# Optimization experiments

Measured on AMD Instinct MI355X. Metric: run time of the kernel, lower is better.

## Reference

```python
import jax, jax.numpy as jnp
import numpy as np
from jax.ops import segment_sum, segment_max

N, E, G = 20000, 100000, 16
TILE, EMB, HID, OUT, FEAT, HEADS = 32, 128, 256, 512, 512, 8
SLOPE = 0.2


def setup_inputs() -> dict:
    key = jax.random.key(0)
    ks = jax.random.split(key, 20)
    def gn(k, shape, fan_in):
        return jax.random.normal(k, shape, jnp.float32) * (1.0 / np.sqrt(fan_in))
    return {
        "x": jax.random.normal(ks[0], (N, TILE), jnp.float32),
        "edge_index": jax.random.randint(ks[1], (2, E), 0, N, jnp.int32),
        "batch": jnp.sort(jax.random.randint(ks[2], (N,), 0, G, jnp.int32)),
        "W0": gn(ks[3], (TILE, EMB), TILE), "b0": jnp.zeros((EMB,), jnp.float32),
        "W1": gn(ks[4], (EMB, HEADS * HID), EMB),
        "a1s": gn(ks[5], (HEADS, HID), HID), "a1d": gn(ks[6], (HEADS, HID), HID),
        "b1": jnp.zeros((HEADS * HID,), jnp.float32),
        "W2": gn(ks[7], (HEADS * HID, HEADS * HID), HEADS * HID),
        "a2s": gn(ks[8], (HEADS, HID), HID), "a2d": gn(ks[9], (HEADS, HID), HID),
        "b2": jnp.zeros((HEADS * HID,), jnp.float32),
        "W3": gn(ks[10], (HEADS * HID, OUT), HEADS * HID),
        "a3s": gn(ks[11], (1, OUT), OUT), "a3d": gn(ks[12], (1, OUT), OUT),
        "b3": jnp.zeros((OUT,), jnp.float32),
        "Wf": gn(ks[13], (OUT, FEAT), OUT), "bf": jnp.zeros((FEAT,), jnp.float32),
    }


def gat_conv(x, src, dst, W, a_s, a_d, b, heads, ch, n):
    # PyG GATConv: linear, per-edge additive attention, segment softmax over dst, scatter-add
    h = (x @ W).reshape(n, heads, ch)                       # [N,H,C]
    e_src = jnp.einsum("nhc,hc->nh", h, a_s)                 # [N,H]
    e_dst = jnp.einsum("nhc,hc->nh", h, a_d)
    e = jax.nn.leaky_relu(e_src[src] + e_dst[dst], SLOPE)    # [E,H]
    m = segment_max(e, dst, num_segments=n)                  # [N,H]
    m = jax.lax.stop_gradient(jnp.where(jnp.isfinite(m), m, 0.0))
    ex = jnp.exp(e - m[dst])
    den = segment_sum(ex, dst, num_segments=n)
    alpha = ex / (den[dst] + 1e-16)                          # [E,H]
    out = segment_sum(h[src] * alpha[..., None], dst, num_segments=n)  # [N,H,C]
    return out.reshape(n, heads * ch) + b


def reference(x, edge_index, batch, W0, b0, W1, a1s, a1d, b1, W2, a2s, a2d, b2,
              W3, a3s, a3d, b3, Wf, bf):
    loop = jnp.arange(N, dtype=edge_index.dtype)             # PyG adds self-loops by default
    src = jnp.concatenate([edge_index[0], loop])
    dst = jnp.concatenate([edge_index[1], loop])
    h = jax.nn.leaky_relu(x @ W0 + b0, SLOPE)
    h = jax.nn.leaky_relu(gat_conv(h, src, dst, W1, a1s, a1d, b1, HEADS, HID, N), SLOPE)
    h = jax.nn.leaky_relu(gat_conv(h, src, dst, W2, a2s, a2d, b2, HEADS, HID, N), SLOPE)
    h = jax.nn.leaky_relu(gat_conv(h, src, dst, W3, a3s, a3d, b3, 1, OUT, N), SLOPE)
    sums = segment_sum(h, batch, num_segments=G)             # global_mean_pool
    cnt = segment_sum(jnp.ones((N,), h.dtype), batch, num_segments=G)
    mean = sums / jnp.maximum(cnt, 1.0)[:, None]
    return jax.nn.leaky_relu(mean @ Wf + bf, SLOPE)
```

## Files before the change

### kernel.cpp

```cpp
#include <hip/hip_runtime.h>
#include <hip/hip_bf16.h>

#define N_NODES 20000
#define N_EDGES 100000
#define ET (N_EDGES + N_NODES)
#define G_GRAPHS 16
#define SLOPE 0.2f

using short8  = __attribute__((ext_vector_type(8))) short;
using floatx4 = __attribute__((ext_vector_type(4))) float;

__device__ __forceinline__ float lrelu(float x) { return x > 0.f ? x : SLOPE * x; }

__device__ __forceinline__ float b2f(unsigned short u) {
    union { unsigned int i; float f; } v; v.i = ((unsigned int)u) << 16; return v.f;
}
__device__ __forceinline__ unsigned short f2b(float f) {
    union { float f; unsigned int i; } v; v.f = f;
    unsigned int i = v.i;
    return (unsigned short)((i + 0x7fffu + ((i >> 16) & 1u)) >> 16);
}

__device__ __forceinline__ void gld16(const void* g, void* l) {
    __builtin_amdgcn_global_load_lds((const __attribute__((address_space(1))) void*)g,
                                     (__attribute__((address_space(3))) void*)l, 16, 0, 0);
}

__device__ int dev_lower_bound(const int* a, int n, int key) {
    int lo = 0, hi = n;
    while (lo < hi) { int mid = (lo + hi) >> 1; if (a[mid] < key) lo = mid + 1; else hi = mid; }
    return lo;
}

__global__ void zero_kernel(int* __restrict__ p, int n) {
    int i = blockIdx.x * blockDim.x + threadIdx.x;
    if (i < n) p[i] = 0;
}

__global__ void count_kernel(const int* __restrict__ ei, int* __restrict__ counts) {
    int e = blockIdx.x * blockDim.x + threadIdx.x;
    if (e >= ET) return;
    int dst = (e < N_EDGES) ? ei[N_EDGES + e] : (e - N_EDGES);
    atomicAdd(&counts[dst], 1);
}

__global__ void scan_kernel(const int* __restrict__ counts, int* __restrict__ row_ptr) {
    __shared__ int sums[256];
    int t = threadIdx.x;
    const int CH = (N_NODES + 255) / 256;
    int base = t * CH;
    int s = 0;
    for (int i = 0; i < CH; i++) { int idx = base + i; if (idx < N_NODES) s += counts[idx]; }
    sums[t] = s;
    __syncthreads();
    for (int off = 1; off < 256; off <<= 1) {
        int v = (t >= off) ? sums[t - off] : 0;
        __syncthreads();
        sums[t] += v;
        __syncthreads();
    }
    int run = (t == 0) ? 0 : sums[t - 1];
    for (int i = 0; i < CH; i++) {
        int idx = base + i;
        if (idx < N_NODES) { row_ptr[idx] = run; run += counts[idx]; }
    }
    if (t == 255) row_ptr[N_NODES] = run;
}

__global__ void fill_kernel(const int* __restrict__ ei, const int* __restrict__ row_ptr,
                            int* __restrict__ fill_cnt, int* __restrict__ col) {
    int e = blockIdx.x * blockDim.x + threadIdx.x;
    if (e >= ET) return;
    int src, dst;
    if (e < N_EDGES) { src = ei[e]; dst = ei[N_EDGES + e]; }
    else             { src = dst = e - N_EDGES; }
    int pos = atomicAdd(&fill_cnt[dst], 1);
    col[row_ptr[dst] + pos] = src;
}

__global__ void transpose_kernel(const float* __restrict__ W, unsigned short* __restrict__ Wt,
                                 int K, int N) {
    __shared__ float tile[32][33];
    int bn = blockIdx.x * 32, bk = blockIdx.y * 32;
    int tx = threadIdx.x & 31, ty = threadIdx.x >> 5;
#pragma unroll
    for (int p = 0; p < 32; p += 8)
        tile[ty + p][tx] = W[(size_t)(bk + ty + p) * N + bn + tx];
    __syncthreads();
#pragma unroll
    for (int p = 0; p < 32; p += 8)
        Wt[(size_t)(bn + ty + p) * K + bk + tx] = f2b(tile[tx][ty + p]);
}

__global__ void gemm0_kernel(const float* __restrict__ x, const float* __restrict__ W0,
                             const float* __restrict__ b0, unsigned short* __restrict__ h0) {
    __shared__ float xr[32];
    int n = blockIdx.x, t = threadIdx.x;
    if (t < 32) xr[t] = x[n * 32 + t];
    __syncthreads();
    float acc = 0.f;
#pragma unroll
    for (int k = 0; k < 32; k++) acc += xr[k] * W0[k * 128 + t];
    h0[(size_t)n * 128 + t] = f2b(lrelu(acc + b0[t]));
}

__global__ void wes_kernel(const float* __restrict__ W1, const float* __restrict__ a1s,
                           const float* __restrict__ a1d, float* __restrict__ w_es,
                           float* __restrict__ w_ed) {
    int hd = blockIdx.x;
    int k  = threadIdx.x;
    const float* w  = W1 + (size_t)k * 2048 + hd * 256;
    const float* as_ = a1s + hd * 256;
    const float* ad_ = a1d + hd * 256;
    float s1 = 0.f, s2 = 0.f;
    for (int c = 0; c < 256; c++) { float wv = w[c]; s1 += wv * as_[c]; s2 += wv * ad_[c]; }
    w_es[k * 8 + hd] = s1;
    w_ed[k * 8 + hd] = s2;
}

__global__ void es1_kernel(const unsigned short* __restrict__ h0, const float* __restrict__ w_es,
                           const float* __restrict__ w_ed, float* __restrict__ es,
                           float* __restrict__ ed) {
    int n = blockIdx.x, t = threadIdx.x;
    int hd = t >> 5, l = t & 31;
    uint2 u = *(const uint2*)&h0[(size_t)n * 128 + l * 4];
    float x0 = b2f((unsigned short)(u.x & 0xffff)), x1 = b2f((unsigned short)(u.x >> 16));
    float x2 = b2f((unsigned short)(u.y & 0xffff)), x3 = b2f((unsigned short)(u.y >> 16));
    int k0 = l * 4;
    float s1 = x0 * w_es[(k0 + 0) * 8 + hd] + x1 * w_es[(k0 + 1) * 8 + hd] +
               x2 * w_es[(k0 + 2) * 8 + hd] + x3 * w_es[(k0 + 3) * 8 + hd];
    float s2 = x0 * w_ed[(k0 + 0) * 8 + hd] + x1 * w_ed[(k0 + 1) * 8 + hd] +
               x2 * w_ed[(k0 + 2) * 8 + hd] + x3 * w_ed[(k0 + 3) * 8 + hd];
    for (int m = 16; m >= 1; m >>= 1) { s1 += __shfl_xor(s1, m); s2 += __shfl_xor(s2, m); }
    if (l == 0) { es[n * 8 + hd] = s1; ed[n * 8 + hd] = s2; }
}

__global__ __launch_bounds__(256) void agg1_wave(const unsigned short* __restrict__ h0,
                                                 const float* __restrict__ es,
                                                 const float* __restrict__ ed,
                                                 const int* __restrict__ row_ptr,
                                                 const int* __restrict__ col,
                                                 unsigned short* __restrict__ outp) {
    int wv = threadIdx.x >> 6, l = threadIdx.x & 63;
    int v = blockIdx.x * 4 + wv;
    if (v >= N_NODES) return;
    int rs = row_ptr[v], deg = row_ptr[v + 1] - rs;
    float edv[8], den[8], a0[8], a1[8];
#pragma unroll
    for (int hd = 0; hd < 8; hd++) { edv[hd] = ed[v * 8 + hd]; den[hd] = 0.f; a0[hd] = 0.f; a1[hd] = 0.f; }
    int sN = (deg > 0) ? col[rs] : 0;
    for (int e = 0; e < deg; e++) {
        int s = sN;
        if (e + 1 < deg) sN = col[rs + e + 1];
        unsigned int u = *(const unsigned int*)&h0[(size_t)s * 128 + l * 2];
        float x0 = b2f((unsigned short)(u & 0xffff)), x1 = b2f((unsigned short)(u >> 16));
#pragma unroll
        for (int hd = 0; hd < 8; hd++) {
            float a = __expf(lrelu(es[s * 8 + hd] + edv[hd]));
            den[hd] += a;
            a0[hd] += a * x0;
            a1[hd] += a * x1;
        }
    }
#pragma unroll
    for (int hd = 0; hd < 8; hd++) {
        float inv = 1.f / (den[hd] + 1e-16f);
        unsigned int o = (unsigned int)f2b(a0[hd] * inv) | ((unsigned int)f2b(a1[hd] * inv) << 16);
        *(unsigned int*)&outp[(size_t)v * 1024 + hd * 128 + l * 2] = o;
    }
}

__global__ __launch_bounds__(256) void gemm_mfma(const unsigned short* __restrict__ A,
                                                 const unsigned short* __restrict__ Bt,
                                                 unsigned short* __restrict__ C,
                                                 int M, int N, int K) {
    __shared__ __align__(16) unsigned short As[128][32];
    __shared__ __align__(16) unsigned short Bs[128][32];
    int t = threadIdx.x;
    int w = t >> 6, l = t & 63;
    int r0 = blockIdx.y * 128, c0 = blockIdx.x * 128;
    int wr = (w >> 1) * 64, wc = (w & 1) * 64;
    int lrow = l >> 2;
    int gcb  = (l & 3) ^ ((l >> 3) & 3);
    int m16 = l & 15, qb = l >> 4;
    int sw  = (m16 >> 1) & 3;
    int roff = ((qb ^ sw) * 8);
    floatx4 acc[4][4] = {};

    for (int k0 = 0; k0 < K; k0 += 32) {
        __syncthreads();
#pragma unroll
        for (int q = 0; q < 2; q++) {
            int row = w * 32 + q * 16 + lrow;
            int ga = min(r0 + row, M - 1);
            gld16(A + (size_t)ga * K + k0 + gcb * 8, &As[w * 32 + q * 16][0]);
            gld16(Bt + (size_t)(c0 + row) * K + k0 + gcb * 8, &Bs[w * 32 + q * 16][0]);
        }
        __syncthreads();
        short8 af[4], bfr[4];
#pragma unroll
        for (int i = 0; i < 4; i++) af[i] = *(const short8*)&As[wr + i * 16 + m16][roff];
#pragma unroll
        for (int j = 0; j < 4; j++) bfr[j] = *(const short8*)&Bs[wc + j * 16 + m16][roff];
#pragma unroll
        for (int i = 0; i < 4; i++)
#pragma unroll
            for (int j = 0; j < 4; j++)
                acc[i][j] = __builtin_amdgcn_mfma_f32_16x16x32_bf16(bfr[j], af[i], acc[i][j], 0, 0, 0);
    }
    int quad = l >> 4;
#pragma unroll
    for (int i = 0; i < 4; i++) {
        int r = r0 + wr + i * 16 + m16;
        if (r < M) {
#pragma unroll
            for (int j = 0; j < 4; j++) {
                int c = c0 + wc + j * 16 + quad * 4;
                ushort4 o = make_ushort4(f2b(acc[i][j][0]), f2b(acc[i][j][1]),
                                         f2b(acc[i][j][2]), f2b(acc[i][j][3]));
                *(ushort4*)&C[(size_t)r * N + c] = o;
            }
        }
    }
}

__global__ __launch_bounds__(256) void gemm_mfma_h1(const unsigned short* __restrict__ A,
                                                    const unsigned short* __restrict__ Bt,
                                                    const float* __restrict__ bias,
                                                    unsigned short* __restrict__ C,
                                                    int M) {
    const int N = 2048, K = 128;
    __shared__ __align__(16) unsigned short As[128][32];
    __shared__ __align__(16) unsigned short Bs[128][32];
    int t = threadIdx.x;
    int w = t >> 6, l = t & 63;
    int r0 = blockIdx.y * 128, c0 = blockIdx.x * 128;
    int wr = (w >> 1) * 64, wc = (w & 1) * 64;
    int lrow = l >> 2;
    int gcb  = (l & 3) ^ ((l >> 3) & 3);
    int m16 = l & 15, qb = l >> 4;
    int sw  = (m16 >> 1) & 3;
    int roff = ((qb ^ sw) * 8);
    int aoff = (c0 >> 8) * 128;
    floatx4 acc[4][4] = {};

    for (int k0 = 0; k0 < K; k0 += 32) {
        __syncthreads();
#pragma unroll
        for (int q = 0; q < 2; q++) {
            int row = w * 32 + q * 16 + lrow;
            int ga = min(r0 + row, M - 1);
            gld16(A + (size_t)ga * 1024 + aoff + k0 + gcb * 8, &As[w * 32 + q * 16][0]);
            gld16(Bt + (size_t)(c0 + row) * K + k0 + gcb * 8, &Bs[w * 32 + q * 16][0]);
        }
        __syncthreads();
        short8 af[4], bfr[4];
#pragma unroll
        for (int i = 0; i < 4; i++) af[i] = *(const short8*)&As[wr + i * 16 + m16][roff];
#pragma unroll
        for (int j = 0; j < 4; j++) bfr[j] = *(const short8*)&Bs[wc + j * 16 + m16][roff];
#pragma unroll
        for (int i = 0; i < 4; i++)
#pragma unroll
            for (int j = 0; j < 4; j++)
                acc[i][j] = __builtin_amdgcn_mfma_f32_16x16x32_bf16(bfr[j], af[i], acc[i][j], 0, 0, 0);
    }
    int quad = l >> 4;
#pragma unroll
    for (int i = 0; i < 4; i++) {
        int r = r0 + wr + i * 16 + m16;
        if (r < M) {
#pragma unroll
            for (int j = 0; j < 4; j++) {
                int c = c0 + wc + j * 16 + quad * 4;
                ushort4 o = make_ushort4(f2b(lrelu(acc[i][j][0] + bias[c + 0])),
                                         f2b(lrelu(acc[i][j][1] + bias[c + 1])),
                                         f2b(lrelu(acc[i][j][2] + bias[c + 2])),
                                         f2b(lrelu(acc[i][j][3] + bias[c + 3])));
                *(ushort4*)&C[(size_t)r * N + c] = o;
            }
        }
    }
}

__global__ void att8_kernel(const unsigned short* __restrict__ h, const float* __restrict__ a_s,
                            const float* __restrict__ a_d, float* __restrict__ es,
                            float* __restrict__ ed) {
    int n = blockIdx.x, t = threadIdx.x;
    int hd = t >> 5, l = t & 31;
    const unsigned short* hr = h + (size_t)n * 2048 + hd * 256 + l * 8;
    const float* as_ = a_s + hd * 256 + l * 8;
    const float* ad_ = a_d + hd * 256 + l * 8;
    uint4 u = *(const uint4*)hr;
    float v[8] = { b2f((unsigned short)(u.x & 0xffff)), b2f((unsigned short)(u.x >> 16)),
                   b2f((unsigned short)(u.y & 0xffff)), b2f((unsigned short)(u.y >> 16)),
                   b2f((unsigned short)(u.z & 0xffff)), b2f((unsigned short)(u.z >> 16)),
                   b2f((unsigned short)(u.w & 0xffff)), b2f((unsigned short)(u.w >> 16)) };
    float s1 = 0.f, s2 = 0.f;
#pragma unroll
    for (int j = 0; j < 8; j++) { s1 += v[j] * as_[j]; s2 += v[j] * ad_[j]; }
    for (int m = 16; m >= 1; m >>= 1) { s1 += __shfl_xor(s1, m); s2 += __shfl_xor(s2, m); }
    if (l == 0) { es[n * 8 + hd] = s1; ed[n * 8 + hd] = s2; }
}

__global__ void att1_kernel(const unsigned short* __restrict__ h, const float* __restrict__ a_s,
                            const float* __restrict__ a_d, float* __restrict__ es,
                            float* __restrict__ ed) {
    int n = blockIdx.x, l = threadIdx.x;
    const unsigned short* hr = h + (size_t)n * 512 + l * 8;
    const float* as_ = a_s + l * 8;
    const float* ad_ = a_d + l * 8;
    uint4 u = *(const uint4*)hr;
    float v[8] = { b2f((unsigned short)(u.x & 0xffff)), b2f((unsigned short)(u.x >> 16)),
                   b2f((unsigned short)(u.y & 0xffff)), b2f((unsigned short)(u.y >> 16)),
                   b2f((unsigned short)(u.z & 0xffff)), b2f((unsigned short)(u.z >> 16)),
                   b2f((unsigned short)(u.w & 0xffff)), b2f((unsigned short)(u.w >> 16)) };
    float s1 = 0.f, s2 = 0.f;
#pragma unroll
    for (int j = 0; j < 8; j++) { s1 += v[j] * as_[j]; s2 += v[j] * ad_[j]; }
    for (int m = 32; m >= 1; m >>= 1) { s1 += __shfl_xor(s1, m); s2 += __shfl_xor(s2, m); }
    if (l == 0) { es[n] = s1; ed[n] = s2; }
}

template <int H, int C>
__global__ __launch_bounds__(256) void agg_wave(const unsigned short* __restrict__ hmid,
                                                const float* __restrict__ es,
                                                const float* __restrict__ ed,
                                                const int* __restrict__ row_ptr,
                                                const int* __restrict__ col,
                                                const float* __restrict__ bias,
                                                unsigned short* __restrict__ out) {
    constexpr int HC = H * C;
    constexpr int CH = HC / 512;
    int wv = threadIdx.x >> 6, l = threadIdx.x & 63;
    int v = blockIdx.x * 4 + wv;
    if (v >= N_NODES) return;
    int rs = row_ptr[v], deg = row_ptr[v + 1] - rs;
    int hd[CH];
    float edv[CH], den[CH], acc[CH][8];
#pragma unroll
    for (int c = 0; c < CH; c++) {
        hd[c] = (c * 512 + l * 8) / C;
        edv[c] = ed[v * H + hd[c]];
        den[c] = 0.f;
#pragma unroll
        for (int k = 0; k < 8; k++) acc[c][k] = 0.f;
    }
    int sN = (deg > 0) ? col[rs] : 0;
    for (int e = 0; e < deg; e++) {
        int s = sN;
        if (e + 1 < deg) sN = col[rs + e + 1];
        const unsigned short* hr = hmid + (size_t)s * HC + l * 8;
        uint4 u[CH];
#pragma unroll
        for (int c = 0; c < CH; c++) u[c] = *(const uint4*)(hr + c * 512);
        float ex[CH];
#pragma unroll
        for (int c = 0; c < CH; c++) {
            ex[c] = __expf(lrelu(es[s * H + hd[c]] + edv[c]));
            den[c] += ex[c];
        }
#pragma unroll
        for (int c = 0; c < CH; c++) {
            float a = ex[c];
            acc[c][0] += a * b2f((unsigned short)(u[c].x & 0xffff));
            acc[c][1] += a * b2f((unsigned short)(u[c].x >> 16));
            acc[c][2] += a * b2f((unsigned short)(u[c].y & 0xffff));
            acc[c][3] += a * b2f((unsigned short)(u[c].y >> 16));
            acc[c][4] += a * b2f((unsigned short)(u[c].z & 0xffff));
            acc[c][5] += a * b2f((unsigned short)(u[c].z >> 16));
            acc[c][6] += a * b2f((unsigned short)(u[c].w & 0xffff));
            acc[c][7] += a * b2f((unsigned short)(u[c].w >> 16));
        }
    }
#pragma unroll
    for (int c = 0; c < CH; c++) {
        float inv = 1.f / (den[c] + 1e-16f);
        unsigned short o[8];
#pragma unroll
        for (int k = 0; k < 8; k++)
            o[k] = f2b(lrelu(acc[c][k] * inv + bias[c * 512 + l * 8 + k]));
        *(uint4*)&out[(size_t)v * HC + c * 512 + l * 8] = *(const uint4*)o;
    }
}

__global__ void pool_kernel(const unsigned short* __restrict__ h3, const int* __restrict__ batch,
                            float* __restrict__ msum) {
    int b0 = blockIdx.x * 128, t = threadIdx.x;
    int nend = min(b0 + 128, N_NODES);
    int curg = batch[b0];
    float s0 = 0.f, s1 = 0.f;
    for (int n = b0; n < nend; n++) {
        int g = batch[n];
        if (g != curg) {
            atomicAdd(&msum[curg * 512 + t * 2], s0);
            atomicAdd(&msum[curg * 512 + t * 2 + 1], s1);
            s0 = s1 = 0.f; curg = g;
        }
        unsigned int u = *(const unsigned int*)&h3[(size_t)n * 512 + t * 2];
        s0 += b2f((unsigned short)(u & 0xffff));
        s1 += b2f((unsigned short)(u >> 16));
    }
    atomicAdd(&msum[curg * 512 + t * 2], s0);
    atomicAdd(&msum[curg * 512 + t * 2 + 1], s1);
}

__global__ void final_kernel(const float* __restrict__ msum, const int* __restrict__ batch,
                             const float* __restrict__ Wf, const float* __restrict__ bf,
                             float* __restrict__ out) {
    int g = blockIdx.x, t = threadIdx.x;
    __shared__ float mr[512];
    __shared__ float sinv;
    if (t == 0) {
        int st = dev_lower_bound(batch, N_NODES, g);
        int en = dev_lower_bound(batch, N_NODES, g + 1);
        sinv = 1.f / fmaxf((float)(en - st), 1.f);
    }
    __syncthreads();
    for (int c = t; c < 512; c += 256) mr[c] = msum[g * 512 + c] * sinv;
    __syncthreads();
    for (int j = t; j < 512; j += 256) {
        float s = 0.f;
        for (int k = 0; k < 512; k++) s += mr[k] * Wf[k * 512 + j];
        out[g * 512 + j] = lrelu(s + bf[j]);
    }
}

extern "C" void kernel_launch(void* const* d_in, const int* in_sizes, int n_in,
                              void* d_out, int out_size, void* d_ws, size_t ws_size,
                              hipStream_t stream) {
    const float* x   = (const float*)d_in[0];
    const int*   ei  = (const int*)d_in[1];
    const int*   bat = (const int*)d_in[2];
    const float* W0  = (const float*)d_in[3];
    const float* b0  = (const float*)d_in[4];
    const float* W1  = (const float*)d_in[5];
    const float* a1s = (const float*)d_in[6];
    const float* a1d = (const float*)d_in[7];
    const float* b1  = (const float*)d_in[8];
    const float* W2  = (const float*)d_in[9];
    const float* a2s = (const float*)d_in[10];
    const float* a2d = (const float*)d_in[11];
    const float* b2  = (const float*)d_in[12];
    const float* W3  = (const float*)d_in[13];
    const float* a3s = (const float*)d_in[14];
    const float* a3d = (const float*)d_in[15];
    const float* b3  = (const float*)d_in[16];
    const float* Wf  = (const float*)d_in[17];
    const float* bf  = (const float*)d_in[18];
    float* out = (float*)d_out;

    char* p = (char*)d_ws;
    unsigned short* bufA = (unsigned short*)p; p += (size_t)N_NODES * 2048 * 2;
    unsigned short* bufB = (unsigned short*)p; p += (size_t)N_NODES * 2048 * 2;
    unsigned short* h0   = (unsigned short*)p; p += (size_t)N_NODES * 128 * 2;
    unsigned short* W1t  = (unsigned short*)p; p += (size_t)2048 * 128 * 2;
    unsigned short* W2t  = (unsigned short*)p; p += (size_t)2048 * 2048 * 2;
    unsigned short* W3t  = (unsigned short*)p; p += (size_t)512 * 2048 * 2;
    float* es   = (float*)p; p += (size_t)N_NODES * 8 * 4;
    float* ed   = (float*)p; p += (size_t)N_NODES * 8 * 4;
    float* w_es = (float*)p; p += 128 * 8 * 4;
    float* w_ed = (float*)p; p += 128 * 8 * 4;
    float* msum = (float*)p; p += 16 * 512 * 4;
    int* counts  = (int*)p; p += (size_t)N_NODES * 4;
    int* row_ptr = (int*)p; p += (size_t)(N_NODES + 1) * 4;
    int* col     = (int*)p; p += (size_t)ET * 4;

    zero_kernel<<<(N_NODES + 255) / 256, 256, 0, stream>>>(counts, N_NODES);
    count_kernel<<<(ET + 255) / 256, 256, 0, stream>>>(ei, counts);
    scan_kernel<<<1, 256, 0, stream>>>(counts, row_ptr);
    zero_kernel<<<(N_NODES + 255) / 256, 256, 0, stream>>>(counts, N_NODES);
    fill_kernel<<<(ET + 255) / 256, 256, 0, stream>>>(ei, row_ptr, counts, col);

    transpose_kernel<<<dim3(2048 / 32, 128 / 32), 256, 0, stream>>>(W1, W1t, 128, 2048);
    transpose_kernel<<<dim3(2048 / 32, 2048 / 32), 256, 0, stream>>>(W2, W2t, 2048, 2048);
    transpose_kernel<<<dim3(512 / 32, 2048 / 32), 256, 0, stream>>>(W3, W3t, 2048, 512);

    wes_kernel<<<8, 128, 0, stream>>>(W1, a1s, a1d, w_es, w_ed);

    zero_kernel<<<(16 * 512 + 255) / 256, 256, 0, stream>>>((int*)msum, 16 * 512);

    gemm0_kernel<<<N_NODES, 128, 0, stream>>>(x, W0, b0, h0);

    dim3 g12(2048 / 128, (N_NODES + 127) / 128);
    dim3 g3(512 / 128, (N_NODES + 127) / 128);
    int aggb = (N_NODES + 3) / 4;

    es1_kernel<<<N_NODES, 256, 0, stream>>>(h0, w_es, w_ed, es, ed);
    agg1_wave<<<aggb, 256, 0, stream>>>(h0, es, ed, row_ptr, col, bufB);
    gemm_mfma_h1<<<g12, 256, 0, stream>>>(bufB, W1t, b1, bufA, N_NODES);

    gemm_mfma<<<g12, 256, 0, stream>>>(bufA, W2t, bufB, N_NODES, 2048, 2048);
    att8_kernel<<<N_NODES, 256, 0, stream>>>(bufB, a2s, a2d, es, ed);
    agg_wave<8, 256><<<aggb, 256, 0, stream>>>(bufB, es, ed, row_ptr, col, b2, bufA);

    gemm_mfma<<<g3, 256, 0, stream>>>(bufA, W3t, bufB, N_NODES, 512, 2048);
    att1_kernel<<<N_NODES, 64, 0, stream>>>(bufB, a3s, a3d, es, ed);
    agg_wave<1, 512><<<aggb, 256, 0, stream>>>(bufB, es, ed, row_ptr, col, b3, bufA);

    pool_kernel<<<(N_NODES + 127) / 128, 256, 0, stream>>>(bufA, bat, msum);
    final_kernel<<<G_GRAPHS, 256, 0, stream>>>(msum, bat, Wf, bf, out);
}
```

Before: 828.5 us.

## Fuse prep kernels, deepen GEMM K-tile to 64, unroll aggregation by two edges

Merges the three weight transposes and the attention-weight precompute into one launch. Folds the layer-1 attention score computation into the input embedding kernel, and folds the counts reset into the scan. GEMMs now stage 64-wide K slices with an 8-way XOR swizzle, halving the barrier count per tile. The aggregation loop processes two edges per iteration to raise memory-level parallelism, and pooling plus the final linear layer become one kernel. The cost is that pooling now runs on only 16 blocks, each serially summing about 1250 rows, and the GEMMs use more shared memory per block.

```diff
diff --git a/kernel.cpp b/kernel.cpp
--- a/kernel.cpp
+++ b/kernel.cpp
@@ -44,7 +44,7 @@
     atomicAdd(&counts[dst], 1);
 }
 
-__global__ void scan_kernel(const int* __restrict__ counts, int* __restrict__ row_ptr) {
+__global__ void scan_kernel(int* __restrict__ counts, int* __restrict__ row_ptr) {
     __shared__ int sums[256];
     int t = threadIdx.x;
     const int CH = (N_NODES + 255) / 256;
@@ -62,7 +62,12 @@
     int run = (t == 0) ? 0 : sums[t - 1];
     for (int i = 0; i < CH; i++) {
         int idx = base + i;
-        if (idx < N_NODES) { row_ptr[idx] = run; run += counts[idx]; }
+        if (idx < N_NODES) {
+            int c = counts[idx];
+            row_ptr[idx] = run;
+            run += c;
+            counts[idx] = 0;
+        }
     }
     if (t == 255) row_ptr[N_NODES] = run;
 }
@@ -78,10 +83,31 @@
     col[row_ptr[dst] + pos] = src;
 }
 
-__global__ void transpose_kernel(const float* __restrict__ W, unsigned short* __restrict__ Wt,
-                                 int K, int N) {
+__global__ void prep_kernel(const float* __restrict__ W1, const float* __restrict__ W2,
+                            const float* __restrict__ W3, const float* __restrict__ a1s,
+                            const float* __restrict__ a1d, unsigned short* __restrict__ W1t,
+                            unsigned short* __restrict__ W2t, unsigned short* __restrict__ W3t,
+                            float* __restrict__ w_es, float* __restrict__ w_ed) {
+    int z = blockIdx.z;
+    if (z == 3) {
+        if (blockIdx.x >= 8 || blockIdx.y > 0 || threadIdx.x >= 128) return;
+        int hd = blockIdx.x, k = threadIdx.x;
+        const float* w   = W1 + (size_t)k * 2048 + hd * 256;
+        const float* as_ = a1s + hd * 256;
+        const float* ad_ = a1d + hd * 256;
+        float s1 = 0.f, s2 = 0.f;
+        for (int c = 0; c < 256; c++) { float wv = w[c]; s1 += wv * as_[c]; s2 += wv * ad_[c]; }
+        w_es[k * 8 + hd] = s1;
+        w_ed[k * 8 + hd] = s2;
+        return;
+    }
+    const float* W; unsigned short* Wt; int K, N;
+    if (z == 0)      { W = W1; Wt = W1t; K = 128;  N = 2048; }
+    else if (z == 1) { W = W2; Wt = W2t; K = 2048; N = 2048; }
+    else             { W = W3; Wt = W3t; K = 2048; N = 512;  }
+    int bn = blockIdx.x * 32, bk = blockIdx.y * 32;
+    if (bn >= N || bk >= K) return;
     __shared__ float tile[32][33];
-    int bn = blockIdx.x * 32, bk = blockIdx.y * 32;
     int tx = threadIdx.x & 31, ty = threadIdx.x >> 5;
 #pragma unroll
     for (int p = 0; p < 32; p += 8)
@@ -92,47 +118,37 @@
         Wt[(size_t)(bn + ty + p) * K + bk + tx] = f2b(tile[tx][ty + p]);
 }
 
-__global__ void gemm0_kernel(const float* __restrict__ x, const float* __restrict__ W0,
-                             const float* __restrict__ b0, unsigned short* __restrict__ h0) {
+__global__ void gemm0es_kernel(const float* __restrict__ x, const float* __restrict__ W0,
+                               const float* __restrict__ b0, const float* __restrict__ w_es,
+                               const float* __restrict__ w_ed, unsigned short* __restrict__ h0,
+                               float* __restrict__ es, float* __restrict__ ed) {
     __shared__ float xr[32];
+    __shared__ float red[2][16];
     int n = blockIdx.x, t = threadIdx.x;
     if (t < 32) xr[t] = x[n * 32 + t];
     __syncthreads();
     float acc = 0.f;
 #pragma unroll
     for (int k = 0; k < 32; k++) acc += xr[k] * W0[k * 128 + t];
-    h0[(size_t)n * 128 + t] = f2b(lrelu(acc + b0[t]));
-}
-
-__global__ void wes_kernel(const float* __restrict__ W1, const float* __restrict__ a1s,
-                           const float* __restrict__ a1d, float* __restrict__ w_es,
-                           float* __restrict__ w_ed) {
-    int hd = blockIdx.x;
-    int k  = threadIdx.x;
-    const float* w  = W1 + (size_t)k * 2048 + hd * 256;
-    const float* as_ = a1s + hd * 256;
-    const float* ad_ = a1d + hd * 256;
-    float s1 = 0.f, s2 = 0.f;
-    for (int c = 0; c < 256; c++) { float wv = w[c]; s1 += wv * as_[c]; s2 += wv * ad_[c]; }
-    w_es[k * 8 + hd] = s1;
-    w_ed[k * 8 + hd] = s2;
-}
-
-__global__ void es1_kernel(const unsigned short* __restrict__ h0, const float* __restrict__ w_es,
-                           const float* __restrict__ w_ed, float* __restrict__ es,
-                           float* __restrict__ ed) {
-    int n = blockIdx.x, t = threadIdx.x;
-    int hd = t >> 5, l = t & 31;
-    uint2 u = *(const uint2*)&h0[(size_t)n * 128 + l * 4];
-    float x0 = b2f((unsigned short)(u.x & 0xffff)), x1 = b2f((unsigned short)(u.x >> 16));
-    float x2 = b2f((unsigned short)(u.y & 0xffff)), x3 = b2f((unsigned short)(u.y >> 16));
-    int k0 = l * 4;
-    float s1 = x0 * w_es[(k0 + 0) * 8 + hd] + x1 * w_es[(k0 + 1) * 8 + hd] +
-               x2 * w_es[(k0 + 2) * 8 + hd] + x3 * w_es[(k0 + 3) * 8 + hd];
-    float s2 = x0 * w_ed[(k0 + 0) * 8 + hd] + x1 * w_ed[(k0 + 1) * 8 + hd] +
-               x2 * w_ed[(k0 + 2) * 8 + hd] + x3 * w_ed[(k0 + 3) * 8 + hd];
-    for (int m = 16; m >= 1; m >>= 1) { s1 += __shfl_xor(s1, m); s2 += __shfl_xor(s2, m); }
-    if (l == 0) { es[n * 8 + hd] = s1; ed[n * 8 + hd] = s2; }
+    float h = lrelu(acc + b0[t]);
+    h0[(size_t)n * 128 + t] = f2b(h);
+    float p[16];
+#pragma unroll
+    for (int hd = 0; hd < 8; hd++) {
+        p[hd]     = h * w_es[t * 8 + hd];
+        p[8 + hd] = h * w_ed[t * 8 + hd];
+    }
+#pragma unroll
+    for (int m = 1; m < 64; m <<= 1)
+#pragma unroll
+        for (int i = 0; i < 16; i++) p[i] += __shfl_xor(p[i], m);
+    int w = t >> 6, l = t & 63;
+    if (l == 0)
+#pragma unroll
+        for (int i = 0; i < 16; i++) red[w][i] = p[i];
+    __syncthreads();
+    if (t < 8)       es[n * 8 + t] = red[0][t] + red[1][t];
+    else if (t < 16) ed[n * 8 + (t - 8)] = red[0][t] + red[1][t];
 }
 
 __global__ __launch_bounds__(256) void agg1_wave(const unsigned short* __restrict__ h0,
@@ -174,39 +190,41 @@
                                                  const unsigned short* __restrict__ Bt,
                                                  unsigned short* __restrict__ C,
                                                  int M, int N, int K) {
-    __shared__ __align__(16) unsigned short As[128][32];
-    __shared__ __align__(16) unsigned short Bs[128][32];
+    __shared__ __align__(16) unsigned short As[128][64];
+    __shared__ __align__(16) unsigned short Bs[128][64];
     int t = threadIdx.x;
     int w = t >> 6, l = t & 63;
     int r0 = blockIdx.y * 128, c0 = blockIdx.x * 128;
     int wr = (w >> 1) * 64, wc = (w & 1) * 64;
-    int lrow = l >> 2;
-    int gcb  = (l & 3) ^ ((l >> 3) & 3);
+    int srow = l >> 3;
+    int gcb  = (l & 7) ^ srow;
     int m16 = l & 15, qb = l >> 4;
-    int sw  = (m16 >> 1) & 3;
-    int roff = ((qb ^ sw) * 8);
     floatx4 acc[4][4] = {};
 
-    for (int k0 = 0; k0 < K; k0 += 32) {
+    for (int k0 = 0; k0 < K; k0 += 64) {
         __syncthreads();
 #pragma unroll
-        for (int q = 0; q < 2; q++) {
-            int row = w * 32 + q * 16 + lrow;
+        for (int q = 0; q < 4; q++) {
+            int row = w * 32 + q * 8 + srow;
             int ga = min(r0 + row, M - 1);
-            gld16(A + (size_t)ga * K + k0 + gcb * 8, &As[w * 32 + q * 16][0]);
-            gld16(Bt + (size_t)(c0 + row) * K + k0 + gcb * 8, &Bs[w * 32 + q * 16][0]);
+            gld16(A + (size_t)ga * K + k0 + gcb * 8, &As[w * 32 + q * 8][0]);
+            gld16(Bt + (size_t)(c0 + row) * K + k0 + gcb * 8, &Bs[w * 32 + q * 8][0]);
         }
         __syncthreads();
-        short8 af[4], bfr[4];
-#pragma unroll
-        for (int i = 0; i < 4; i++) af[i] = *(const short8*)&As[wr + i * 16 + m16][roff];
-#pragma unroll
-        for (int j = 0; j < 4; j++) bfr[j] = *(const short8*)&Bs[wc + j * 16 + m16][roff];
-#pragma unroll
-        for (int i = 0; i < 4; i++)
-#pragma unroll
-            for (int j = 0; j < 4; j++)
-                acc[i][j] = __builtin_amdgcn_mfma_f32_16x16x32_bf16(bfr[j], af[i], acc[i][j], 0, 0, 0);
+#pragma unroll
+        for (int kh = 0; kh < 2; kh++) {
+            int roff = (((kh * 4 + qb) ^ (m16 & 7)) * 8);
+            short8 af[4], bfr[4];
+#pragma unroll
+            for (int i = 0; i < 4; i++) af[i] = *(const short8*)&As[wr + i * 16 + m16][roff];
+#pragma unroll
+            for (int j = 0; j < 4; j++) bfr[j] = *(const short8*)&Bs[wc + j * 16 + m16][roff];
+#pragma unroll
+            for (int i = 0; i < 4; i++)
+#pragma unroll
+                for (int j = 0; j < 4; j++)
+                    acc[i][j] = __builtin_amdgcn_mfma_f32_16x16x32_bf16(bfr[j], af[i], acc[i][j], 0, 0, 0);
+        }
     }
     int quad = l >> 4;
 #pragma unroll
@@ -230,40 +248,42 @@
                                                     unsigned short* __restrict__ C,
                                                     int M) {
     const int N = 2048, K = 128;
-    __shared__ __align__(16) unsigned short As[128][32];
-    __shared__ __align__(16) unsigned short Bs[128][32];
+    __shared__ __align__(16) unsigned short As[128][64];
+    __shared__ __align__(16) unsigned short Bs[128][64];
     int t = threadIdx.x;
     int w = t >> 6, l = t & 63;
     int r0 = blockIdx.y * 128, c0 = blockIdx.x * 128;
     int wr = (w >> 1) * 64, wc = (w & 1) * 64;
-    int lrow = l >> 2;
-    int gcb  = (l & 3) ^ ((l >> 3) & 3);
+    int srow = l >> 3;
+    int gcb  = (l & 7) ^ srow;
     int m16 = l & 15, qb = l >> 4;
-    int sw  = (m16 >> 1) & 3;
-    int roff = ((qb ^ sw) * 8);
     int aoff = (c0 >> 8) * 128;
     floatx4 acc[4][4] = {};
 
-    for (int k0 = 0; k0 < K; k0 += 32) {
+    for (int k0 = 0; k0 < K; k0 += 64) {
         __syncthreads();
 #pragma unroll
-        for (int q = 0; q < 2; q++) {
-            int row = w * 32 + q * 16 + lrow;
+        for (int q = 0; q < 4; q++) {
+            int row = w * 32 + q * 8 + srow;
             int ga = min(r0 + row, M - 1);
-            gld16(A + (size_t)ga * 1024 + aoff + k0 + gcb * 8, &As[w * 32 + q * 16][0]);
-            gld16(Bt + (size_t)(c0 + row) * K + k0 + gcb * 8, &Bs[w * 32 + q * 16][0]);
+            gld16(A + (size_t)ga * 1024 + aoff + k0 + gcb * 8, &As[w * 32 + q * 8][0]);
+            gld16(Bt + (size_t)(c0 + row) * K + k0 + gcb * 8, &Bs[w * 32 + q * 8][0]);
         }
         __syncthreads();
-        short8 af[4], bfr[4];
-#pragma unroll
-        for (int i = 0; i < 4; i++) af[i] = *(const short8*)&As[wr + i * 16 + m16][roff];
-#pragma unroll
-        for (int j = 0; j < 4; j++) bfr[j] = *(const short8*)&Bs[wc + j * 16 + m16][roff];
-#pragma unroll
-        for (int i = 0; i < 4; i++)
-#pragma unroll
-            for (int j = 0; j < 4; j++)
-                acc[i][j] = __builtin_amdgcn_mfma_f32_16x16x32_bf16(bfr[j], af[i], acc[i][j], 0, 0, 0);
+#pragma unroll
+        for (int kh = 0; kh < 2; kh++) {
+            int roff = (((kh * 4 + qb) ^ (m16 & 7)) * 8);
+            short8 af[4], bfr[4];
+#pragma unroll
+            for (int i = 0; i < 4; i++) af[i] = *(const short8*)&As[wr + i * 16 + m16][roff];
+#pragma unroll
+            for (int j = 0; j < 4; j++) bfr[j] = *(const short8*)&Bs[wc + j * 16 + m16][roff];
+#pragma unroll
+            for (int i = 0; i < 4; i++)
+#pragma unroll
+                for (int j = 0; j < 4; j++)
+                    acc[i][j] = __builtin_amdgcn_mfma_f32_16x16x32_bf16(bfr[j], af[i], acc[i][j], 0, 0, 0);
+        }
     }
     int quad = l >> 4;
 #pragma unroll
@@ -346,31 +366,50 @@
 #pragma unroll
         for (int k = 0; k < 8; k++) acc[c][k] = 0.f;
     }
-    int sN = (deg > 0) ? col[rs] : 0;
-    for (int e = 0; e < deg; e++) {
-        int s = sN;
-        if (e + 1 < deg) sN = col[rs + e + 1];
+    int e = 0;
+    for (; e + 2 <= deg; e += 2) {
+        int s0 = col[rs + e], s1 = col[rs + e + 1];
+        const unsigned short* hr0 = hmid + (size_t)s0 * HC + l * 8;
+        const unsigned short* hr1 = hmid + (size_t)s1 * HC + l * 8;
+        uint4 u0[CH], u1[CH];
+#pragma unroll
+        for (int c = 0; c < CH; c++) { u0[c] = *(const uint4*)(hr0 + c * 512); u1[c] = *(const uint4*)(hr1 + c * 512); }
+        float ex0[CH], ex1[CH];
+#pragma unroll
+        for (int c = 0; c < CH; c++) {
+            ex0[c] = __expf(lrelu(es[s0 * H + hd[c]] + edv[c]));
+            ex1[c] = __expf(lrelu(es[s1 * H + hd[c]] + edv[c]));
+            den[c] += ex0[c] + ex1[c];
+        }
+#pragma unroll
+        for (int c = 0; c < CH; c++) {
+            float a = ex0[c], b = ex1[c];
+            acc[c][0] += a * b2f((unsigned short)(u0[c].x & 0xffff)) + b * b2f((unsigned short)(u1[c].x & 0xffff));
+            acc[c][1] += a * b2f((unsigned short)(u0[c].x >> 16))    + b * b2f((unsigned short)(u1[c].x >> 16));
+            acc[c][2] += a * b2f((unsigned short)(u0[c].y & 0xffff)) + b * b2f((unsigned short)(u1[c].y & 0xffff));
+            acc[c][3] += a * b2f((unsigned short)(u0[c].y >> 16))    + b * b2f((unsigned short)(u1[c].y >> 16));
+            acc[c][4] += a * b2f((unsigned short)(u0[c].z & 0xffff)) + b * b2f((unsigned short)(u1[c].z & 0xffff));
+            acc[c][5] += a * b2f((unsigned short)(u0[c].z >> 16))    + b * b2f((unsigned short)(u1[c].z >> 16));
+            acc[c][6] += a * b2f((unsigned short)(u0[c].w & 0xffff)) + b * b2f((unsigned short)(u1[c].w & 0xffff));
+            acc[c][7] += a * b2f((unsigned short)(u0[c].w >> 16))    + b * b2f((unsigned short)(u1[c].w >> 16));
+        }
+    }
+    if (e < deg) {
+        int s = col[rs + e];
         const unsigned short* hr = hmid + (size_t)s * HC + l * 8;
-        uint4 u[CH];
-#pragma unroll
-        for (int c = 0; c < CH; c++) u[c] = *(const uint4*)(hr + c * 512);
-        float ex[CH];
 #pragma unroll
         for (int c = 0; c < CH; c++) {
-            ex[c] = __expf(lrelu(es[s * H + hd[c]] + edv[c]));
-            den[c] += ex[c];
-        }
-#pragma unroll
-        for (int c = 0; c < CH; c++) {
-            float a = ex[c];
-            acc[c][0] += a * b2f((unsigned short)(u[c].x & 0xffff));
-            acc[c][1] += a * b2f((unsigned short)(u[c].x >> 16));
-            acc[c][2] += a * b2f((unsigned short)(u[c].y & 0xffff));
-            acc[c][3] += a * b2f((unsigned short)(u[c].y >> 16));
-            acc[c][4] += a * b2f((unsigned short)(u[c].z & 0xffff));
-            acc[c][5] += a * b2f((unsigned short)(u[c].z >> 16));
-            acc[c][6] += a * b2f((unsigned short)(u[c].w & 0xffff));
-            acc[c][7] += a * b2f((unsigned short)(u[c].w >> 16));
+            uint4 u = *(const uint4*)(hr + c * 512);
+            float a = __expf(lrelu(es[s * H + hd[c]] + edv[c]));
+            den[c] += a;
+            acc[c][0] += a * b2f((unsigned short)(u.x & 0xffff));
+            acc[c][1] += a * b2f((unsigned short)(u.x >> 16));
+            acc[c][2] += a * b2f((unsigned short)(u.y & 0xffff));
+            acc[c][3] += a * b2f((unsigned short)(u.y >> 16));
+            acc[c][4] += a * b2f((unsigned short)(u.z & 0xffff));
+            acc[c][5] += a * b2f((unsigned short)(u.z >> 16));
+            acc[c][6] += a * b2f((unsigned short)(u.w & 0xffff));
+            acc[c][7] += a * b2f((unsigned short)(u.w >> 16));
         }
     }
 #pragma unroll
@@ -384,46 +423,22 @@
     }
 }
 
-__global__ void pool_kernel(const unsigned short* __restrict__ h3, const int* __restrict__ batch,
-                            float* __restrict__ msum) {
-    int b0 = blockIdx.x * 128, t = threadIdx.x;
-    int nend = min(b0 + 128, N_NODES);
-    int curg = batch[b0];
-    float s0 = 0.f, s1 = 0.f;
-    for (int n = b0; n < nend; n++) {
-        int g = batch[n];
-        if (g != curg) {
-            atomicAdd(&msum[curg * 512 + t * 2], s0);
-            atomicAdd(&msum[curg * 512 + t * 2 + 1], s1);
-            s0 = s1 = 0.f; curg = g;
-        }
-        unsigned int u = *(const unsigned int*)&h3[(size_t)n * 512 + t * 2];
-        s0 += b2f((unsigned short)(u & 0xffff));
-        s1 += b2f((unsigned short)(u >> 16));
-    }
-    atomicAdd(&msum[curg * 512 + t * 2], s0);
-    atomicAdd(&msum[curg * 512 + t * 2 + 1], s1);
-}
-
-__global__ void final_kernel(const float* __restrict__ msum, const int* __restrict__ batch,
-                             const float* __restrict__ Wf, const float* __restrict__ bf,
-                             float* __restrict__ out) {
+__global__ __launch_bounds__(512) void poolfinal_kernel(const unsigned short* __restrict__ h3,
+                                                        const int* __restrict__ batch,
+                                                        const float* __restrict__ Wf,
+                                                        const float* __restrict__ bf,
+                                                        float* __restrict__ out) {
     int g = blockIdx.x, t = threadIdx.x;
     __shared__ float mr[512];
-    __shared__ float sinv;
-    if (t == 0) {
-        int st = dev_lower_bound(batch, N_NODES, g);
-        int en = dev_lower_bound(batch, N_NODES, g + 1);
-        sinv = 1.f / fmaxf((float)(en - st), 1.f);
-    }
+    int st = dev_lower_bound(batch, N_NODES, g);
+    int en = dev_lower_bound(batch, N_NODES, g + 1);
+    float s = 0.f;
+    for (int n = st; n < en; n++) s += b2f(h3[(size_t)n * 512 + t]);
+    mr[t] = s * (1.f / fmaxf((float)(en - st), 1.f));
     __syncthreads();
-    for (int c = t; c < 512; c += 256) mr[c] = msum[g * 512 + c] * sinv;
-    __syncthreads();
-    for (int j = t; j < 512; j += 256) {
-        float s = 0.f;
-        for (int k = 0; k < 512; k++) s += mr[k] * Wf[k * 512 + j];
-        out[g * 512 + j] = lrelu(s + bf[j]);
-    }
+    float o = 0.f;
+    for (int k = 0; k < 512; k++) o += mr[k] * Wf[k * 512 + t];
+    out[g * 512 + t] = lrelu(o + bf[t]);
 }
 
 extern "C" void kernel_launch(void* const* d_in, const int* in_sizes, int n_in,
@@ -461,7 +476,6 @@
     float* ed   = (float*)p; p += (size_t)N_NODES * 8 * 4;
     float* w_es = (float*)p; p += 128 * 8 * 4;
     float* w_ed = (float*)p; p += 128 * 8 * 4;
-    float* msum = (float*)p; p += 16 * 512 * 4;
     int* counts  = (int*)p; p += (size_t)N_NODES * 4;
     int* row_ptr = (int*)p; p += (size_t)(N_NODES + 1) * 4;
     int* col     = (int*)p; p += (size_t)ET * 4;
@@ -469,24 +483,17 @@
     zero_kernel<<<(N_NODES + 255) / 256, 256, 0, stream>>>(counts, N_NODES);
     count_kernel<<<(ET + 255) / 256, 256, 0, stream>>>(ei, counts);
     scan_kernel<<<1, 256, 0, stream>>>(counts, row_ptr);
-    zero_kernel<<<(N_NODES + 255) / 256, 256, 0, stream>>>(counts, N_NODES);
     fill_kernel<<<(ET + 255) / 256, 256, 0, stream>>>(ei, row_ptr, counts, col);
 
-    transpose_kernel<<<dim3(2048 / 32, 128 / 32), 256, 0, stream>>>(W1, W1t, 128, 2048);
-    transpose_kernel<<<dim3(2048 / 32, 2048 / 32), 256, 0, stream>>>(W2, W2t, 2048, 2048);
-    transpose_kernel<<<dim3(512 / 32, 2048 / 32), 256, 0, stream>>>(W3, W3t, 2048, 512);
-
-    wes_kernel<<<8, 128, 0, stream>>>(W1, a1s, a1d, w_es, w_ed);
-
-    zero_kernel<<<(16 * 512 + 255) / 256, 256, 0, stream>>>((int*)msum, 16 * 512);
-
-    gemm0_kernel<<<N_NODES, 128, 0, stream>>>(x, W0, b0, h0);
+    prep_kernel<<<dim3(64, 64, 4), 256, 0, stream>>>(W1, W2, W3, a1s, a1d,
+                                                     W1t, W2t, W3t, w_es, w_ed);
+
+    gemm0es_kernel<<<N_NODES, 128, 0, stream>>>(x, W0, b0, w_es, w_ed, h0, es, ed);
 
     dim3 g12(2048 / 128, (N_NODES + 127) / 128);
     dim3 g3(512 / 128, (N_NODES + 127) / 128);
     int aggb = (N_NODES + 3) / 4;
 
-    es1_kernel<<<N_NODES, 256, 0, stream>>>(h0, w_es, w_ed, es, ed);
     agg1_wave<<<aggb, 256, 0, stream>>>(h0, es, ed, row_ptr, col, bufB);
     gemm_mfma_h1<<<g12, 256, 0, stream>>>(bufB, W1t, b1, bufA, N_NODES);
 
@@ -498,6 +505,5 @@
     att1_kernel<<<N_NODES, 64, 0, stream>>>(bufB, a3s, a3d, es, ed);
     agg_wave<1, 512><<<aggb, 256, 0, stream>>>(bufB, es, ed, row_ptr, col, b3, bufA);
 
-    pool_kernel<<<(N_NODES + 127) / 128, 256, 0, stream>>>(bufA, bat, msum);
-    final_kernel<<<G_GRAPHS, 256, 0, stream>>>(msum, bat, Wf, bf, out);
-}
+    poolfinal_kernel<<<G_GRAPHS, 512, 0, stream>>>(bufA, bat, Wf, bf, out);
+}
```

New measurement: 1.035 ms. +24.9%, slower.
